# Performance work log

Measured on AMD Instinct MI355X. Metric: run time of the kernel, lower is better.

Reference implementation:

```python
import jax, jax.numpy as jnp
import numpy as np

N_NODES = 50000
N_EDGES = 800000


def setup_inputs() -> dict:
    key = jax.random.key(0)
    ks = jax.random.split(key, 9)
    d, h, hd = 128, 4, 32
    s = 1.0 / np.sqrt(d)
    return {
        "x": jax.random.normal(ks[0], (N_NODES, d), jnp.float32),
        "edge_index": jax.random.randint(ks[1], (2, N_EDGES), 0, N_NODES, jnp.int32),
        "W0": jax.random.normal(ks[2], (d, d), jnp.float32) * s,
        "att_l0": jax.random.normal(ks[3], (h, hd), jnp.float32) * s,
        "att_r0": jax.random.normal(ks[4], (h, hd), jnp.float32) * s,
        "b0": jnp.zeros((d,), jnp.float32),
        "W1": jax.random.normal(ks[5], (d, d), jnp.float32) * s,
        "att_l1": jax.random.normal(ks[6], (h, hd), jnp.float32) * s,
        "att_r1": jax.random.normal(ks[7], (h, hd), jnp.float32) * s,
        "b1": jnp.zeros((hd,), jnp.float32),
    }


def _gat_layer(x, src, dst, W, att_l, att_r, bias, concat):
    # x: [N, F_in]; W: [H*D, F_in] (torch Linear layout); att_*: [H, D]
    n = x.shape[0]
    h, d = att_l.shape
    hx = (x @ W.T).reshape(n, h, d)                     # [N,H,D]
    al = jnp.einsum('nhd,hd->nh', hx, att_l)            # [N,H]
    ar = jnp.einsum('nhd,hd->nh', hx, att_r)
    att = al[src] + ar[dst]                             # [E,H]
    att = jax.nn.leaky_relu(att, negative_slope=0.2)
    # segment softmax over destination nodes
    m = jax.ops.segment_max(att, dst, num_segments=n)   # [N,H]
    att = jnp.exp(att - m[dst])
    ssum = jax.ops.segment_sum(att, dst, num_segments=n)
    att = att / (ssum[dst] + 1e-9)                      # [E,H]
    msgs = att[:, :, None] * hx[src]                    # [E,H,D]
    out = jax.ops.segment_sum(msgs, dst, num_segments=n)  # [N,H,D]
    if concat:
        out = out.reshape(n, h * d)
    else:
        out = out.mean(axis=1)
    return out + bias


def reference(x, edge_index, W0, att_l0, att_r0, b0, W1, att_l1, att_r1, b1):
    src, dst = edge_index[0], edge_index[1]
    x = _gat_layer(x, src, dst, W0, att_l0, att_r0, b0, concat=True)
    x = jax.nn.relu(x)  # dropout is identity in eval mode
    x = _gat_layer(x, src, dst, W1, att_l1, att_r1, b1, concat=False)
    return x
```

## Files before the change

kernel.cpp:

```cpp
#include <hip/hip_runtime.h>
#include <hip/hip_bf16.h>

#define H 4
#define D 32
#define F 128
#define MAXDEG 64
#define PF 16

typedef __attribute__((ext_vector_type(8))) short bf16x8;
typedef __attribute__((ext_vector_type(4))) float f32x4;

__device__ __forceinline__ short f2bf(float v) {
    __hip_bfloat16 h = __float2bfloat16(v);
    return *reinterpret_cast<short*>(&h);
}
__device__ __forceinline__ float bf2f(short s) {
    __hip_bfloat16 h = *reinterpret_cast<__hip_bfloat16*>(&s);
    return __bfloat162float(h);
}

__device__ __forceinline__
void gemm_body(int bid, int nblocks, const float* __restrict__ X,
               const float* __restrict__ W, const float* __restrict__ attl,
               const float* __restrict__ attr, __hip_bfloat16* __restrict__ HXB,
               float* __restrict__ AL, float* __restrict__ AR, int ntiles) {
    const int wave = threadIdx.x >> 6;
    const int lane = threadIdx.x & 63;
    const int m    = lane & 15;
    const int q    = lane >> 4;
    const int q8   = q * 8;

    bf16x8 Bhi[2][4], Blo[2][4];
#pragma unroll
    for (int j = 0; j < 2; ++j) {
        const int fout = wave * 32 + j * 16 + m;
#pragma unroll
        for (int kc = 0; kc < 4; ++kc) {
            const float* wp = W + (size_t)fout * F + kc * 32 + q8;
            float4 w0 = *reinterpret_cast<const float4*>(wp);
            float4 w1 = *reinterpret_cast<const float4*>(wp + 4);
            float wv[8] = {w0.x, w0.y, w0.z, w0.w, w1.x, w1.y, w1.z, w1.w};
#pragma unroll
            for (int t = 0; t < 8; ++t) {
                short h = f2bf(wv[t]);
                Bhi[j][kc][t] = h;
                Blo[j][kc][t] = f2bf(wv[t] - bf2f(h));
            }
        }
    }
    const float alw0  = attl[wave * 32 + m];
    const float alw16 = attl[wave * 32 + 16 + m];
    const float arw0  = attr[wave * 32 + m];
    const float arw16 = attr[wave * 32 + 16 + m];

    for (int tile = bid; tile < ntiles; tile += nblocks) {
        const int node0 = tile * 16;
        bf16x8 Ahi[4], Alo[4];
        const float* xp = X + (size_t)(node0 + m) * F + q8;
#pragma unroll
        for (int kc = 0; kc < 4; ++kc) {
            float4 x0 = *reinterpret_cast<const float4*>(xp + kc * 32);
            float4 x1 = *reinterpret_cast<const float4*>(xp + kc * 32 + 4);
            float xv[8] = {x0.x, x0.y, x0.z, x0.w, x1.x, x1.y, x1.z, x1.w};
#pragma unroll
            for (int t = 0; t < 8; ++t) {
                short h = f2bf(xv[t]);
                Ahi[kc][t] = h;
                Alo[kc][t] = f2bf(xv[t] - bf2f(h));
            }
        }
        f32x4 acc0 = {0.f, 0.f, 0.f, 0.f};
        f32x4 acc1 = {0.f, 0.f, 0.f, 0.f};
#pragma unroll
        for (int kc = 0; kc < 4; ++kc) {
            acc0 = __builtin_amdgcn_mfma_f32_16x16x32_bf16(Ahi[kc], Bhi[0][kc], acc0, 0, 0, 0);
            acc1 = __builtin_amdgcn_mfma_f32_16x16x32_bf16(Ahi[kc], Bhi[1][kc], acc1, 0, 0, 0);
            acc0 = __builtin_amdgcn_mfma_f32_16x16x32_bf16(Ahi[kc], Blo[0][kc], acc0, 0, 0, 0);
            acc1 = __builtin_amdgcn_mfma_f32_16x16x32_bf16(Ahi[kc], Blo[1][kc], acc1, 0, 0, 0);
            acc0 = __builtin_amdgcn_mfma_f32_16x16x32_bf16(Alo[kc], Bhi[0][kc], acc0, 0, 0, 0);
            acc1 = __builtin_amdgcn_mfma_f32_16x16x32_bf16(Alo[kc], Bhi[1][kc], acc1, 0, 0, 0);
        }
        const int row0 = node0 + q * 4;
        const int col0 = wave * 32 + m;
#pragma unroll
        for (int r = 0; r < 4; ++r) {
            HXB[(size_t)(row0 + r) * F + col0]      = __float2bfloat16(acc0[r]);
            HXB[(size_t)(row0 + r) * F + col0 + 16] = __float2bfloat16(acc1[r]);
            float pal = acc0[r] * alw0 + acc1[r] * alw16;
            float par = acc0[r] * arw0 + acc1[r] * arw16;
#pragma unroll
            for (int o = 1; o < 16; o <<= 1) {
                pal += __shfl_xor(pal, o);
                par += __shfl_xor(par, o);
            }
            if (m == 0) {
                AL[(size_t)(row0 + r) * H + wave] = pal;
                AR[(size_t)(row0 + r) * H + wave] = par;
            }
        }
    }
}

__device__ __forceinline__
void wconv_body(const float* __restrict__ W1, __hip_bfloat16* __restrict__ W1hi,
                __hip_bfloat16* __restrict__ W1lo) {
    for (int i = threadIdx.x; i < F * F; i += 256) {
        float v = W1[i];
        short hi = f2bf(v);
        *reinterpret_cast<short*>(&W1hi[i]) = hi;
        *reinterpret_cast<short*>(&W1lo[i]) = f2bf(v - bf2f(hi));
    }
}

__device__ __forceinline__
void scatter_body(int sbid, const int* __restrict__ ei, int E,
                  int* __restrict__ deg, unsigned short* __restrict__ ssrc2u) {
    int base = (sbid * 256 + (int)threadIdx.x) * 4;
    if (base + 3 < E) {
        int4 s4 = *reinterpret_cast<const int4*>(ei + base);
        int4 d4 = *reinterpret_cast<const int4*>(ei + E + base);
        int s0 = atomicAdd(&deg[d4.x], 1);
        int s1 = atomicAdd(&deg[d4.y], 1);
        int s2 = atomicAdd(&deg[d4.z], 1);
        int s3 = atomicAdd(&deg[d4.w], 1);
        if (s0 < MAXDEG) ssrc2u[d4.x * MAXDEG + s0] = (unsigned short)s4.x;
        if (s1 < MAXDEG) ssrc2u[d4.y * MAXDEG + s1] = (unsigned short)s4.y;
        if (s2 < MAXDEG) ssrc2u[d4.z * MAXDEG + s2] = (unsigned short)s4.z;
        if (s3 < MAXDEG) ssrc2u[d4.w * MAXDEG + s3] = (unsigned short)s4.w;
    } else {
        for (int e = base; e < E; ++e) {
            int src = ei[e], dst = ei[E + e];
            int s = atomicAdd(&deg[dst], 1);
            if (s < MAXDEG) ssrc2u[dst * MAXDEG + s] = (unsigned short)src;
        }
    }
}

__global__ __launch_bounds__(256)
void k_pre(const float* __restrict__ X, const float* __restrict__ W0,
           const float* __restrict__ attl0, const float* __restrict__ attr0,
           __hip_bfloat16* __restrict__ HXB, float* __restrict__ AL,
           float* __restrict__ AR, int ntiles, int gemm_blocks,
           const float* __restrict__ W1, __hip_bfloat16* __restrict__ W1hi,
           __hip_bfloat16* __restrict__ W1lo,
           const int* __restrict__ ei, int E, int scatter_blocks,
           int* __restrict__ deg, unsigned short* __restrict__ ssrc2u) {
    const int bid = blockIdx.x;
    if (bid & 1) {
        const int s = bid >> 1;
        if (s < scatter_blocks) scatter_body(s, ei, E, deg, ssrc2u);
    } else {
        const int g = bid >> 1;
        if (g < gemm_blocks)
            gemm_body(g, gemm_blocks, X, W0, attl0, attr0, HXB, AL, AR, ntiles);
        else if (g == gemm_blocks)
            wconv_body(W1, W1hi, W1lo);
    }
}

__device__ __forceinline__
int stage_node(int g, int t, int n, const unsigned short* __restrict__ ssrc2u,
               const int* __restrict__ deg, const float* __restrict__ AL,
               const float4 ar4, int (*sidx)[MAXDEG], float (*sw)[MAXDEG][H]) {
    const int cnt  = min(deg[n], MAXDEG);
    const int rcnt = (cnt + PF - 1) & ~(PF - 1);
    if (t < rcnt) {
        if (t < cnt) {
            int s = ssrc2u[n * MAXDEG + t];
            sidx[g][t] = s;
            float4 al4 = *reinterpret_cast<const float4*>(AL + (size_t)s * H);
            float a0 = al4.x + ar4.x; a0 = a0 > 0.f ? a0 : 0.2f * a0;
            float a1 = al4.y + ar4.y; a1 = a1 > 0.f ? a1 : 0.2f * a1;
            float a2 = al4.z + ar4.z; a2 = a2 > 0.f ? a2 : 0.2f * a2;
            float a3 = al4.w + ar4.w; a3 = a3 > 0.f ? a3 : 0.2f * a3;
            sw[g][t][0] = __expf(a0);
            sw[g][t][1] = __expf(a1);
            sw[g][t][2] = __expf(a2);
            sw[g][t][3] = __expf(a3);
        } else {
            sidx[g][t] = 0;
            sw[g][t][0] = 0.f; sw[g][t][1] = 0.f; sw[g][t][2] = 0.f; sw[g][t][3] = 0.f;
        }
    }
    __builtin_amdgcn_wave_barrier();
    return rcnt;
}

__device__ __forceinline__
void gather_node(int g, int t, int h, int rcnt, const __hip_bfloat16* __restrict__ HXB,
                 const int (*sidx)[MAXDEG], const float (*sw)[MAXDEG][H],
                 float& accx, float& accy, float& wsum) {
    for (int base = 0; base < rcnt; base += PF) {
        __hip_bfloat162 v[PF];
#pragma unroll
        for (int j = 0; j < PF; ++j) {
            int s = sidx[g][base + j];
            v[j] = *reinterpret_cast<const __hip_bfloat162*>(HXB + (size_t)s * F + 2 * t);
        }
#pragma unroll
        for (int j = 0; j < PF; ++j) {
            float w = sw[g][base + j][h];
            float2 f = __bfloat1622float2(v[j]);
            accx += w * f.x;
            accy += w * f.y;
            wsum += w;
        }
    }
}

__global__ __launch_bounds__(256)
void k_aggr0(const unsigned short* __restrict__ ssrc2u, const int* __restrict__ deg,
             const float* __restrict__ AL, const float* __restrict__ AR,
             const __hip_bfloat16* __restrict__ HXB, const float* __restrict__ bias,
             float* __restrict__ out, int N) {
    __shared__ int   sidx[4][MAXDEG];
    __shared__ float sw[4][MAXDEG][H];
    const int g = threadIdx.x >> 6;
    const int t = threadIdx.x & 63;
    const int n = blockIdx.x * 4 + g;
    if (n >= N) return;
    const int h = t >> 4;
    const float4 ar4 = *reinterpret_cast<const float4*>(AR + (size_t)n * H);
    int rcnt = stage_node(g, t, n, ssrc2u, deg, AL, ar4, sidx, sw);
    float accx = 0.f, accy = 0.f, wsum = 0.f;
    gather_node(g, t, h, rcnt, HXB, sidx, sw, accx, accy, wsum);
    float inv = 1.f / (wsum + 1e-9f);
    float2 o;
    o.x = fmaxf(accx * inv + bias[2 * t], 0.f);
    o.y = fmaxf(accy * inv + bias[2 * t + 1], 0.f);
    *reinterpret_cast<float2*>(out + (size_t)n * F + 2 * t) = o;
}

__global__ __launch_bounds__(256)
void k_gemm1(const float* __restrict__ X, const __hip_bfloat16* __restrict__ W1hi,
             const __hip_bfloat16* __restrict__ W1lo,
             const float* __restrict__ attl, const float* __restrict__ attr,
             __hip_bfloat16* __restrict__ HXB, float* __restrict__ AL,
             float* __restrict__ AR, int ntiles) {
    const int wave = threadIdx.x >> 6;
    const int lane = threadIdx.x & 63;
    const int m    = lane & 15;
    const int q    = lane >> 4;
    const int q8   = q * 8;

    bf16x8 Bhi[2][4], Blo[2][4];
#pragma unroll
    for (int j = 0; j < 2; ++j) {
        const int fout = wave * 32 + j * 16 + m;
#pragma unroll
        for (int kc = 0; kc < 4; ++kc) {
            Bhi[j][kc] = *reinterpret_cast<const bf16x8*>(W1hi + (size_t)fout * F + kc * 32 + q8);
            Blo[j][kc] = *reinterpret_cast<const bf16x8*>(W1lo + (size_t)fout * F + kc * 32 + q8);
        }
    }
    const float alw0  = attl[wave * 32 + m];
    const float alw16 = attl[wave * 32 + 16 + m];
    const float arw0  = attr[wave * 32 + m];
    const float arw16 = attr[wave * 32 + 16 + m];

    for (int tile = blockIdx.x; tile < ntiles; tile += gridDim.x) {
        const int node0 = tile * 16;
        bf16x8 Ahi[4], Alo[4];
        const float* xp = X + (size_t)(node0 + m) * F + q8;
#pragma unroll
        for (int kc = 0; kc < 4; ++kc) {
            float4 x0 = *reinterpret_cast<const float4*>(xp + kc * 32);
            float4 x1 = *reinterpret_cast<const float4*>(xp + kc * 32 + 4);
            float xv[8] = {x0.x, x0.y, x0.z, x0.w, x1.x, x1.y, x1.z, x1.w};
#pragma unroll
            for (int t = 0; t < 8; ++t) {
                short h = f2bf(xv[t]);
                Ahi[kc][t] = h;
                Alo[kc][t] = f2bf(xv[t] - bf2f(h));
            }
        }
        f32x4 acc0 = {0.f, 0.f, 0.f, 0.f};
        f32x4 acc1 = {0.f, 0.f, 0.f, 0.f};
#pragma unroll
        for (int kc = 0; kc < 4; ++kc) {
            acc0 = __builtin_amdgcn_mfma_f32_16x16x32_bf16(Ahi[kc], Bhi[0][kc], acc0, 0, 0, 0);
            acc1 = __builtin_amdgcn_mfma_f32_16x16x32_bf16(Ahi[kc], Bhi[1][kc], acc1, 0, 0, 0);
            acc0 = __builtin_amdgcn_mfma_f32_16x16x32_bf16(Ahi[kc], Blo[0][kc], acc0, 0, 0, 0);
            acc1 = __builtin_amdgcn_mfma_f32_16x16x32_bf16(Ahi[kc], Blo[1][kc], acc1, 0, 0, 0);
            acc0 = __builtin_amdgcn_mfma_f32_16x16x32_bf16(Alo[kc], Bhi[0][kc], acc0, 0, 0, 0);
            acc1 = __builtin_amdgcn_mfma_f32_16x16x32_bf16(Alo[kc], Bhi[1][kc], acc1, 0, 0, 0);
        }
        const int row0 = node0 + q * 4;
        const int col0 = wave * 32 + m;
#pragma unroll
        for (int r = 0; r < 4; ++r) {
            HXB[(size_t)(row0 + r) * F + col0]      = __float2bfloat16(acc0[r]);
            HXB[(size_t)(row0 + r) * F + col0 + 16] = __float2bfloat16(acc1[r]);
            float pal = acc0[r] * alw0 + acc1[r] * alw16;
            float par = acc0[r] * arw0 + acc1[r] * arw16;
#pragma unroll
            for (int o = 1; o < 16; o <<= 1) {
                pal += __shfl_xor(pal, o);
                par += __shfl_xor(par, o);
            }
            if (m == 0) {
                AL[(size_t)(row0 + r) * H + wave] = pal;
                AR[(size_t)(row0 + r) * H + wave] = par;
            }
        }
    }
}

__global__ __launch_bounds__(256)
void k_aggr1(const unsigned short* __restrict__ ssrc2u, const int* __restrict__ deg,
             const float* __restrict__ AL, const float* __restrict__ AR,
             const __hip_bfloat16* __restrict__ HXB, const float* __restrict__ bias,
             float* __restrict__ out, int N) {
    __shared__ int   sidx[4][MAXDEG];
    __shared__ float sw[4][MAXDEG][H];
    const int g = threadIdx.x >> 6;
    const int t = threadIdx.x & 63;
    const int n = blockIdx.x * 4 + g;
    if (n >= N) return;
    const int h = t >> 4;
    const float4 ar4 = *reinterpret_cast<const float4*>(AR + (size_t)n * H);
    int rcnt = stage_node(g, t, n, ssrc2u, deg, AL, ar4, sidx, sw);
    float accx = 0.f, accy = 0.f, wsum = 0.f;
    gather_node(g, t, h, rcnt, HXB, sidx, sw, accx, accy, wsum);
    float inv = 1.f / (wsum + 1e-9f);
    float vx = accx * inv, vy = accy * inv;
    vx += __shfl_xor(vx, 16); vx += __shfl_xor(vx, 32);
    vy += __shfl_xor(vy, 16); vy += __shfl_xor(vy, 32);
    if (t < 16) {
        float2 o;
        o.x = 0.25f * vx + bias[2 * t];
        o.y = 0.25f * vy + bias[2 * t + 1];
        *reinterpret_cast<float2*>(out + (size_t)n * D + 2 * t) = o;
    }
}

extern "C" void kernel_launch(void* const* d_in, const int* in_sizes, int n_in,
                              void* d_out, int out_size, void* d_ws, size_t ws_size,
                              hipStream_t stream) {
    const float* x     = (const float*)d_in[0];
    const int*   ei    = (const int*)d_in[1];
    const float* W0    = (const float*)d_in[2];
    const float* attl0 = (const float*)d_in[3];
    const float* attr0 = (const float*)d_in[4];
    const float* b0    = (const float*)d_in[5];
    const float* W1    = (const float*)d_in[6];
    const float* attl1 = (const float*)d_in[7];
    const float* attr1 = (const float*)d_in[8];
    const float* b1    = (const float*)d_in[9];

    const int N = in_sizes[0] / F;
    const int E = in_sizes[1] / 2;
    const int ntiles = N / 16;

    char* p = (char*)d_ws;
    __hip_bfloat16* HXB  = (__hip_bfloat16*)p;  p += (size_t)N * F * 2;
    float* X1  = (float*)p;                     p += (size_t)N * F * 4;
    __hip_bfloat16* W1hi = (__hip_bfloat16*)p;  p += (size_t)F * F * 2;
    __hip_bfloat16* W1lo = (__hip_bfloat16*)p;  p += (size_t)F * F * 2;
    float* AL  = (float*)p;                     p += (size_t)N * H * 4;
    float* AR  = (float*)p;                     p += (size_t)N * H * 4;
    unsigned short* ssrc2u = (unsigned short*)p; p += (size_t)N * MAXDEG * 2;
    int* deg = (int*)p;

    hipMemsetAsync(deg, 0, (size_t)N * sizeof(int), stream);

    const int gemm_blocks    = 625;
    const int scatter_blocks = (E / 4 + 255) / 256;
    const int grid_pre = 2 * (scatter_blocks > gemm_blocks + 1 ? scatter_blocks
                                                               : gemm_blocks + 1);

    k_pre<<<grid_pre, 256, 0, stream>>>(x, W0, attl0, attr0, HXB, AL, AR,
                                        ntiles, gemm_blocks, W1, W1hi, W1lo,
                                        ei, E, scatter_blocks, deg, ssrc2u);

    k_aggr0<<<(N + 3) / 4, 256, 0, stream>>>(ssrc2u, deg, AL, AR, HXB, b0, X1, N);

    k_gemm1<<<gemm_blocks, 256, 0, stream>>>(X1, W1hi, W1lo, attl1, attr1,
                                             HXB, AL, AR, ntiles);

    k_aggr1<<<(N + 3) / 4, 256, 0, stream>>>(ssrc2u, deg, AL, AR, HXB, b1,
                                             (float*)d_out, N);
}
```

Baseline: 226.2 us.

## Gather two edges per wave with 8-byte loads and compact pre-kernel grid

The aggregation gather now splits each 64-lane wave into two halves that process alternate edges. Each lane loads 4 bf16 features (8 bytes) instead of 2, and the two halves are combined with a cross-half shuffle. This cuts the number of load instructions and doubles in-flight edges per wave, at the cost of an extra reduction and half the lanes sitting idle at the store. Separately, the fused pre-kernel replaces its interleaved block mapping, which launched idle blocks, with contiguous ranges: scatter blocks first, then GEMM blocks, then the weight-conversion block.

```diff
diff --git a/kernel.cpp b/kernel.cpp
--- a/kernel.cpp
+++ b/kernel.cpp
@@ -146,16 +146,13 @@
            const int* __restrict__ ei, int E, int scatter_blocks,
            int* __restrict__ deg, unsigned short* __restrict__ ssrc2u) {
     const int bid = blockIdx.x;
-    if (bid & 1) {
-        const int s = bid >> 1;
-        if (s < scatter_blocks) scatter_body(s, ei, E, deg, ssrc2u);
-    } else {
-        const int g = bid >> 1;
-        if (g < gemm_blocks)
-            gemm_body(g, gemm_blocks, X, W0, attl0, attr0, HXB, AL, AR, ntiles);
-        else if (g == gemm_blocks)
-            wconv_body(W1, W1hi, W1lo);
-    }
+    if (bid < scatter_blocks)
+        scatter_body(bid, ei, E, deg, ssrc2u);
+    else if (bid < scatter_blocks + gemm_blocks)
+        gemm_body(bid - scatter_blocks, gemm_blocks, X, W0, attl0, attr0,
+                  HXB, AL, AR, ntiles);
+    else
+        wconv_body(W1, W1hi, W1lo);
 }
 
 __device__ __forceinline__
@@ -187,25 +184,40 @@
 }
 
 __device__ __forceinline__
-void gather_node(int g, int t, int h, int rcnt, const __hip_bfloat16* __restrict__ HXB,
-                 const int (*sidx)[MAXDEG], const float (*sw)[MAXDEG][H],
-                 float& accx, float& accy, float& wsum) {
+void gather_node_pair(int g, int t, int rcnt, const __hip_bfloat16* __restrict__ HXB,
+                      const int (*sidx)[MAXDEG], const float (*sw)[MAXDEG][H],
+                      float4& acc, float& wsum) {
+    const int half = t >> 5;
+    const int fl   = t & 31;
+    const int h2   = fl >> 3;
     for (int base = 0; base < rcnt; base += PF) {
-        __hip_bfloat162 v[PF];
-#pragma unroll
-        for (int j = 0; j < PF; ++j) {
-            int s = sidx[g][base + j];
-            v[j] = *reinterpret_cast<const __hip_bfloat162*>(HXB + (size_t)s * F + 2 * t);
-        }
-#pragma unroll
-        for (int j = 0; j < PF; ++j) {
-            float w = sw[g][base + j][h];
-            float2 f = __bfloat1622float2(v[j]);
-            accx += w * f.x;
-            accy += w * f.y;
-            wsum += w;
-        }
-    }
+        float2 v[PF / 2];
+        float  w[PF / 2];
+#pragma unroll
+        for (int j = 0; j < PF / 2; ++j) {
+            int e = base + 2 * j + half;
+            int s = sidx[g][e];
+            v[j] = *reinterpret_cast<const float2*>(HXB + (size_t)s * F + 4 * fl);
+            w[j] = sw[g][e][h2];
+        }
+#pragma unroll
+        for (int j = 0; j < PF / 2; ++j) {
+            __hip_bfloat162 p0 = *reinterpret_cast<__hip_bfloat162*>(&v[j].x);
+            __hip_bfloat162 p1 = *reinterpret_cast<__hip_bfloat162*>(&v[j].y);
+            float2 f0 = __bfloat1622float2(p0);
+            float2 f1 = __bfloat1622float2(p1);
+            acc.x += w[j] * f0.x;
+            acc.y += w[j] * f0.y;
+            acc.z += w[j] * f1.x;
+            acc.w += w[j] * f1.y;
+            wsum  += w[j];
+        }
+    }
+    acc.x += __shfl_xor(acc.x, 32);
+    acc.y += __shfl_xor(acc.y, 32);
+    acc.z += __shfl_xor(acc.z, 32);
+    acc.w += __shfl_xor(acc.w, 32);
+    wsum  += __shfl_xor(wsum, 32);
 }
 
 __global__ __launch_bounds__(256)
@@ -219,16 +231,22 @@
     const int t = threadIdx.x & 63;
     const int n = blockIdx.x * 4 + g;
     if (n >= N) return;
-    const int h = t >> 4;
     const float4 ar4 = *reinterpret_cast<const float4*>(AR + (size_t)n * H);
     int rcnt = stage_node(g, t, n, ssrc2u, deg, AL, ar4, sidx, sw);
-    float accx = 0.f, accy = 0.f, wsum = 0.f;
-    gather_node(g, t, h, rcnt, HXB, sidx, sw, accx, accy, wsum);
-    float inv = 1.f / (wsum + 1e-9f);
-    float2 o;
-    o.x = fmaxf(accx * inv + bias[2 * t], 0.f);
-    o.y = fmaxf(accy * inv + bias[2 * t + 1], 0.f);
-    *reinterpret_cast<float2*>(out + (size_t)n * F + 2 * t) = o;
+    float4 acc = {0.f, 0.f, 0.f, 0.f};
+    float wsum = 0.f;
+    gather_node_pair(g, t, rcnt, HXB, sidx, sw, acc, wsum);
+    if (t < 32) {
+        const int fl = t;
+        float inv = 1.f / (wsum + 1e-9f);
+        float4 b = *reinterpret_cast<const float4*>(bias + 4 * fl);
+        float4 o;
+        o.x = fmaxf(acc.x * inv + b.x, 0.f);
+        o.y = fmaxf(acc.y * inv + b.y, 0.f);
+        o.z = fmaxf(acc.z * inv + b.z, 0.f);
+        o.w = fmaxf(acc.w * inv + b.w, 0.f);
+        *reinterpret_cast<float4*>(out + (size_t)n * F + 4 * fl) = o;
+    }
 }
 
 __global__ __launch_bounds__(256)
@@ -317,20 +335,26 @@
     const int t = threadIdx.x & 63;
     const int n = blockIdx.x * 4 + g;
     if (n >= N) return;
-    const int h = t >> 4;
     const float4 ar4 = *reinterpret_cast<const float4*>(AR + (size_t)n * H);
     int rcnt = stage_node(g, t, n, ssrc2u, deg, AL, ar4, sidx, sw);
-    float accx = 0.f, accy = 0.f, wsum = 0.f;
-    gather_node(g, t, h, rcnt, HXB, sidx, sw, accx, accy, wsum);
+    float4 acc = {0.f, 0.f, 0.f, 0.f};
+    float wsum = 0.f;
+    gather_node_pair(g, t, rcnt, HXB, sidx, sw, acc, wsum);
     float inv = 1.f / (wsum + 1e-9f);
-    float vx = accx * inv, vy = accy * inv;
-    vx += __shfl_xor(vx, 16); vx += __shfl_xor(vx, 32);
-    vy += __shfl_xor(vy, 16); vy += __shfl_xor(vy, 32);
-    if (t < 16) {
-        float2 o;
-        o.x = 0.25f * vx + bias[2 * t];
-        o.y = 0.25f * vy + bias[2 * t + 1];
-        *reinterpret_cast<float2*>(out + (size_t)n * D + 2 * t) = o;
+    float4 v;
+    v.x = acc.x * inv; v.y = acc.y * inv; v.z = acc.z * inv; v.w = acc.w * inv;
+    v.x += __shfl_xor(v.x, 8);  v.y += __shfl_xor(v.y, 8);
+    v.z += __shfl_xor(v.z, 8);  v.w += __shfl_xor(v.w, 8);
+    v.x += __shfl_xor(v.x, 16); v.y += __shfl_xor(v.y, 16);
+    v.z += __shfl_xor(v.z, 16); v.w += __shfl_xor(v.w, 16);
+    if (t < 8) {
+        float4 b = *reinterpret_cast<const float4*>(bias + 4 * t);
+        float4 o;
+        o.x = 0.25f * v.x + b.x;
+        o.y = 0.25f * v.y + b.y;
+        o.z = 0.25f * v.z + b.z;
+        o.w = 0.25f * v.w + b.w;
+        *reinterpret_cast<float4*>(out + (size_t)n * D + 4 * t) = o;
     }
 }
 
@@ -366,12 +390,10 @@
 
     const int gemm_blocks    = 625;
     const int scatter_blocks = (E / 4 + 255) / 256;
-    const int grid_pre = 2 * (scatter_blocks > gemm_blocks + 1 ? scatter_blocks
-                                                               : gemm_blocks + 1);
-
-    k_pre<<<grid_pre, 256, 0, stream>>>(x, W0, attl0, attr0, HXB, AL, AR,
-                                        ntiles, gemm_blocks, W1, W1hi, W1lo,
-                                        ei, E, scatter_blocks, deg, ssrc2u);
+
+    k_pre<<<scatter_blocks + gemm_blocks + 1, 256, 0, stream>>>(
+        x, W0, attl0, attr0, HXB, AL, AR, ntiles, gemm_blocks,
+        W1, W1hi, W1lo, ei, E, scatter_blocks, deg, ssrc2u);
 
     k_aggr0<<<(N + 3) / 4, 256, 0, stream>>>(ssrc2u, deg, AL, AR, HXB, b0, X1, N);
 
```

After: 234.8 us. 1.04x slower.

## Compute source attention logits on the fly from gathered features in aggregation

Applied to the files above, without the earlier changes.

Drops the precomputed AL array. The aggregation kernels now rebuild each edge's source logit by dotting the gathered bf16 feature row with att_l through a 16-lane shuffle reduction, instead of staging AL loads and exp weights in shared memory. This removes the AL writes in both GEMMs and the per-edge AL gather, at the cost of extra shuffles and redundant exp per lane. It also changes the k_pre block assignment from interleaved to contiguous GEMM/wconv/scatter ranges. Source logits now come from bf16-rounded features, which slightly changes numerics.

```diff
diff --git a/kernel.cpp b/kernel.cpp
--- a/kernel.cpp
+++ b/kernel.cpp
@@ -21,9 +21,9 @@
 
 __device__ __forceinline__
 void gemm_body(int bid, int nblocks, const float* __restrict__ X,
-               const float* __restrict__ W, const float* __restrict__ attl,
-               const float* __restrict__ attr, __hip_bfloat16* __restrict__ HXB,
-               float* __restrict__ AL, float* __restrict__ AR, int ntiles) {
+               const float* __restrict__ W, const float* __restrict__ attr,
+               __hip_bfloat16* __restrict__ HXB, float* __restrict__ AR,
+               int ntiles) {
     const int wave = threadIdx.x >> 6;
     const int lane = threadIdx.x & 63;
     const int m    = lane & 15;
@@ -48,8 +48,6 @@
             }
         }
     }
-    const float alw0  = attl[wave * 32 + m];
-    const float alw16 = attl[wave * 32 + 16 + m];
     const float arw0  = attr[wave * 32 + m];
     const float arw16 = attr[wave * 32 + 16 + m];
 
@@ -86,17 +84,12 @@
         for (int r = 0; r < 4; ++r) {
             HXB[(size_t)(row0 + r) * F + col0]      = __float2bfloat16(acc0[r]);
             HXB[(size_t)(row0 + r) * F + col0 + 16] = __float2bfloat16(acc1[r]);
-            float pal = acc0[r] * alw0 + acc1[r] * alw16;
             float par = acc0[r] * arw0 + acc1[r] * arw16;
 #pragma unroll
-            for (int o = 1; o < 16; o <<= 1) {
-                pal += __shfl_xor(pal, o);
+            for (int o = 1; o < 16; o <<= 1)
                 par += __shfl_xor(par, o);
-            }
-            if (m == 0) {
-                AL[(size_t)(row0 + r) * H + wave] = pal;
+            if (m == 0)
                 AR[(size_t)(row0 + r) * H + wave] = par;
-            }
         }
     }
 }
@@ -138,104 +131,88 @@
 
 __global__ __launch_bounds__(256)
 void k_pre(const float* __restrict__ X, const float* __restrict__ W0,
-           const float* __restrict__ attl0, const float* __restrict__ attr0,
-           __hip_bfloat16* __restrict__ HXB, float* __restrict__ AL,
+           const float* __restrict__ attr0, __hip_bfloat16* __restrict__ HXB,
            float* __restrict__ AR, int ntiles, int gemm_blocks,
            const float* __restrict__ W1, __hip_bfloat16* __restrict__ W1hi,
            __hip_bfloat16* __restrict__ W1lo,
-           const int* __restrict__ ei, int E, int scatter_blocks,
+           const int* __restrict__ ei, int E,
            int* __restrict__ deg, unsigned short* __restrict__ ssrc2u) {
     const int bid = blockIdx.x;
-    if (bid & 1) {
-        const int s = bid >> 1;
-        if (s < scatter_blocks) scatter_body(s, ei, E, deg, ssrc2u);
-    } else {
-        const int g = bid >> 1;
-        if (g < gemm_blocks)
-            gemm_body(g, gemm_blocks, X, W0, attl0, attr0, HXB, AL, AR, ntiles);
-        else if (g == gemm_blocks)
-            wconv_body(W1, W1hi, W1lo);
-    }
-}
-
-__device__ __forceinline__
-int stage_node(int g, int t, int n, const unsigned short* __restrict__ ssrc2u,
-               const int* __restrict__ deg, const float* __restrict__ AL,
-               const float4 ar4, int (*sidx)[MAXDEG], float (*sw)[MAXDEG][H]) {
-    const int cnt  = min(deg[n], MAXDEG);
-    const int rcnt = (cnt + PF - 1) & ~(PF - 1);
-    if (t < rcnt) {
-        if (t < cnt) {
-            int s = ssrc2u[n * MAXDEG + t];
-            sidx[g][t] = s;
-            float4 al4 = *reinterpret_cast<const float4*>(AL + (size_t)s * H);
-            float a0 = al4.x + ar4.x; a0 = a0 > 0.f ? a0 : 0.2f * a0;
-            float a1 = al4.y + ar4.y; a1 = a1 > 0.f ? a1 : 0.2f * a1;
-            float a2 = al4.z + ar4.z; a2 = a2 > 0.f ? a2 : 0.2f * a2;
-            float a3 = al4.w + ar4.w; a3 = a3 > 0.f ? a3 : 0.2f * a3;
-            sw[g][t][0] = __expf(a0);
-            sw[g][t][1] = __expf(a1);
-            sw[g][t][2] = __expf(a2);
-            sw[g][t][3] = __expf(a3);
-        } else {
-            sidx[g][t] = 0;
-            sw[g][t][0] = 0.f; sw[g][t][1] = 0.f; sw[g][t][2] = 0.f; sw[g][t][3] = 0.f;
-        }
-    }
-    __builtin_amdgcn_wave_barrier();
-    return rcnt;
-}
-
-__device__ __forceinline__
-void gather_node(int g, int t, int h, int rcnt, const __hip_bfloat16* __restrict__ HXB,
-                 const int (*sidx)[MAXDEG], const float (*sw)[MAXDEG][H],
-                 float& accx, float& accy, float& wsum) {
-    for (int base = 0; base < rcnt; base += PF) {
-        __hip_bfloat162 v[PF];
-#pragma unroll
-        for (int j = 0; j < PF; ++j) {
-            int s = sidx[g][base + j];
-            v[j] = *reinterpret_cast<const __hip_bfloat162*>(HXB + (size_t)s * F + 2 * t);
-        }
-#pragma unroll
-        for (int j = 0; j < PF; ++j) {
-            float w = sw[g][base + j][h];
-            float2 f = __bfloat1622float2(v[j]);
-            accx += w * f.x;
-            accy += w * f.y;
-            wsum += w;
-        }
-    }
-}
-
+    if (bid < gemm_blocks)
+        gemm_body(bid, gemm_blocks, X, W0, attr0, HXB, AR, ntiles);
+    else if (bid == gemm_blocks)
+        wconv_body(W1, W1hi, W1lo);
+    else
+        scatter_body(bid - gemm_blocks - 1, ei, E, deg, ssrc2u);
+}
+
+template<int MODE>
 __global__ __launch_bounds__(256)
-void k_aggr0(const unsigned short* __restrict__ ssrc2u, const int* __restrict__ deg,
-             const float* __restrict__ AL, const float* __restrict__ AR,
-             const __hip_bfloat16* __restrict__ HXB, const float* __restrict__ bias,
-             float* __restrict__ out, int N) {
-    __shared__ int   sidx[4][MAXDEG];
-    __shared__ float sw[4][MAXDEG][H];
+void k_aggr(const unsigned short* __restrict__ ssrc2u, const int* __restrict__ deg,
+            const float* __restrict__ AR, const __hip_bfloat16* __restrict__ HXB,
+            const float* __restrict__ attl, const float* __restrict__ bias,
+            float* __restrict__ out, int N) {
+    __shared__ unsigned short sidx[4][MAXDEG];
     const int g = threadIdx.x >> 6;
     const int t = threadIdx.x & 63;
     const int n = blockIdx.x * 4 + g;
     if (n >= N) return;
     const int h = t >> 4;
+    const float alw0 = attl[2 * t];
+    const float alw1 = attl[2 * t + 1];
     const float4 ar4 = *reinterpret_cast<const float4*>(AR + (size_t)n * H);
-    int rcnt = stage_node(g, t, n, ssrc2u, deg, AL, ar4, sidx, sw);
+    const float arh = (h == 0) ? ar4.x : (h == 1) ? ar4.y : (h == 2) ? ar4.z : ar4.w;
+    const int cnt = min(deg[n], MAXDEG);
+    sidx[g][t] = (t < cnt) ? ssrc2u[n * MAXDEG + t] : (unsigned short)0;
+    __builtin_amdgcn_wave_barrier();
     float accx = 0.f, accy = 0.f, wsum = 0.f;
-    gather_node(g, t, h, rcnt, HXB, sidx, sw, accx, accy, wsum);
+    const int rcnt = (cnt + PF - 1) & ~(PF - 1);
+    for (int base = 0; base < rcnt; base += PF) {
+        float2 v[PF];
+#pragma unroll
+        for (int j = 0; j < PF; ++j) {
+            int s = sidx[g][base + j];
+            v[j] = __bfloat1622float2(
+                *reinterpret_cast<const __hip_bfloat162*>(HXB + (size_t)s * F + 2 * t));
+        }
+#pragma unroll
+        for (int j = 0; j < PF; ++j) {
+            float p = v[j].x * alw0 + v[j].y * alw1;
+            p += __shfl_xor(p, 1);
+            p += __shfl_xor(p, 2);
+            p += __shfl_xor(p, 4);
+            p += __shfl_xor(p, 8);
+            float a = p + arh;
+            a = a > 0.f ? a : 0.2f * a;
+            float w = (base + j < cnt) ? __expf(a) : 0.f;
+            accx += w * v[j].x;
+            accy += w * v[j].y;
+            wsum += w;
+        }
+    }
     float inv = 1.f / (wsum + 1e-9f);
-    float2 o;
-    o.x = fmaxf(accx * inv + bias[2 * t], 0.f);
-    o.y = fmaxf(accy * inv + bias[2 * t + 1], 0.f);
-    *reinterpret_cast<float2*>(out + (size_t)n * F + 2 * t) = o;
+    float vx = accx * inv, vy = accy * inv;
+    if (MODE == 0) {
+        float2 o;
+        o.x = fmaxf(vx + bias[2 * t], 0.f);
+        o.y = fmaxf(vy + bias[2 * t + 1], 0.f);
+        *reinterpret_cast<float2*>(out + (size_t)n * F + 2 * t) = o;
+    } else {
+        vx += __shfl_xor(vx, 16); vx += __shfl_xor(vx, 32);
+        vy += __shfl_xor(vy, 16); vy += __shfl_xor(vy, 32);
+        if (t < 16) {
+            float2 o;
+            o.x = 0.25f * vx + bias[2 * t];
+            o.y = 0.25f * vy + bias[2 * t + 1];
+            *reinterpret_cast<float2*>(out + (size_t)n * D + 2 * t) = o;
+        }
+    }
 }
 
 __global__ __launch_bounds__(256)
 void k_gemm1(const float* __restrict__ X, const __hip_bfloat16* __restrict__ W1hi,
              const __hip_bfloat16* __restrict__ W1lo,
-             const float* __restrict__ attl, const float* __restrict__ attr,
-             __hip_bfloat16* __restrict__ HXB, float* __restrict__ AL,
+             const float* __restrict__ attr, __hip_bfloat16* __restrict__ HXB,
              float* __restrict__ AR, int ntiles) {
     const int wave = threadIdx.x >> 6;
     const int lane = threadIdx.x & 63;
@@ -253,8 +230,6 @@
             Blo[j][kc] = *reinterpret_cast<const bf16x8*>(W1lo + (size_t)fout * F + kc * 32 + q8);
         }
     }
-    const float alw0  = attl[wave * 32 + m];
-    const float alw16 = attl[wave * 32 + 16 + m];
     const float arw0  = attr[wave * 32 + m];
     const float arw16 = attr[wave * 32 + 16 + m];
 
@@ -291,46 +266,13 @@
         for (int r = 0; r < 4; ++r) {
             HXB[(size_t)(row0 + r) * F + col0]      = __float2bfloat16(acc0[r]);
             HXB[(size_t)(row0 + r) * F + col0 + 16] = __float2bfloat16(acc1[r]);
-            float pal = acc0[r] * alw0 + acc1[r] * alw16;
             float par = acc0[r] * arw0 + acc1[r] * arw16;
 #pragma unroll
-            for (int o = 1; o < 16; o <<= 1) {
-                pal += __shfl_xor(pal, o);
+            for (int o = 1; o < 16; o <<= 1)
                 par += __shfl_xor(par, o);
-            }
-            if (m == 0) {
-                AL[(size_t)(row0 + r) * H + wave] = pal;
+            if (m == 0)
                 AR[(size_t)(row0 + r) * H + wave] = par;
-            }
-        }
-    }
-}
-
-__global__ __launch_bounds__(256)
-void k_aggr1(const unsigned short* __restrict__ ssrc2u, const int* __restrict__ deg,
-             const float* __restrict__ AL, const float* __restrict__ AR,
-             const __hip_bfloat16* __restrict__ HXB, const float* __restrict__ bias,
-             float* __restrict__ out, int N) {
-    __shared__ int   sidx[4][MAXDEG];
-    __shared__ float sw[4][MAXDEG][H];
-    const int g = threadIdx.x >> 6;
-    const int t = threadIdx.x & 63;
-    const int n = blockIdx.x * 4 + g;
-    if (n >= N) return;
-    const int h = t >> 4;
-    const float4 ar4 = *reinterpret_cast<const float4*>(AR + (size_t)n * H);
-    int rcnt = stage_node(g, t, n, ssrc2u, deg, AL, ar4, sidx, sw);
-    float accx = 0.f, accy = 0.f, wsum = 0.f;
-    gather_node(g, t, h, rcnt, HXB, sidx, sw, accx, accy, wsum);
-    float inv = 1.f / (wsum + 1e-9f);
-    float vx = accx * inv, vy = accy * inv;
-    vx += __shfl_xor(vx, 16); vx += __shfl_xor(vx, 32);
-    vy += __shfl_xor(vy, 16); vy += __shfl_xor(vy, 32);
-    if (t < 16) {
-        float2 o;
-        o.x = 0.25f * vx + bias[2 * t];
-        o.y = 0.25f * vy + bias[2 * t + 1];
-        *reinterpret_cast<float2*>(out + (size_t)n * D + 2 * t) = o;
+        }
     }
 }
 
@@ -357,7 +299,6 @@
     float* X1  = (float*)p;                     p += (size_t)N * F * 4;
     __hip_bfloat16* W1hi = (__hip_bfloat16*)p;  p += (size_t)F * F * 2;
     __hip_bfloat16* W1lo = (__hip_bfloat16*)p;  p += (size_t)F * F * 2;
-    float* AL  = (float*)p;                     p += (size_t)N * H * 4;
     float* AR  = (float*)p;                     p += (size_t)N * H * 4;
     unsigned short* ssrc2u = (unsigned short*)p; p += (size_t)N * MAXDEG * 2;
     int* deg = (int*)p;
@@ -366,18 +307,17 @@
 
     const int gemm_blocks    = 625;
     const int scatter_blocks = (E / 4 + 255) / 256;
-    const int grid_pre = 2 * (scatter_blocks > gemm_blocks + 1 ? scatter_blocks
-                                                               : gemm_blocks + 1);
-
-    k_pre<<<grid_pre, 256, 0, stream>>>(x, W0, attl0, attr0, HXB, AL, AR,
-                                        ntiles, gemm_blocks, W1, W1hi, W1lo,
-                                        ei, E, scatter_blocks, deg, ssrc2u);
-
-    k_aggr0<<<(N + 3) / 4, 256, 0, stream>>>(ssrc2u, deg, AL, AR, HXB, b0, X1, N);
-
-    k_gemm1<<<gemm_blocks, 256, 0, stream>>>(X1, W1hi, W1lo, attl1, attr1,
-                                             HXB, AL, AR, ntiles);
-
-    k_aggr1<<<(N + 3) / 4, 256, 0, stream>>>(ssrc2u, deg, AL, AR, HXB, b1,
-                                             (float*)d_out, N);
-}
+
+    k_pre<<<gemm_blocks + 1 + scatter_blocks, 256, 0, stream>>>(
+        x, W0, attr0, HXB, AR, ntiles, gemm_blocks,
+        W1, W1hi, W1lo, ei, E, deg, ssrc2u);
+
+    k_aggr<0><<<(N + 3) / 4, 256, 0, stream>>>(ssrc2u, deg, AR, HXB, attl0, b0,
+                                               X1, N);
+
+    k_gemm1<<<gemm_blocks, 256, 0, stream>>>(X1, W1hi, W1lo, attr1, HXB, AR,
+                                             ntiles);
+
+    k_aggr<1><<<(N + 3) / 4, 256, 0, stream>>>(ssrc2u, deg, AR, HXB, attl1, b1,
+                                               (float*)d_out, N);
+}
```

New measurement: 299.9 us. +32.6%, slower.

## Replace global-atomic CSR scatter with two-pass bucketed binning

Applied to the files above, without the earlier changes.

The edge scatter changes from one global atomic per edge on the degree array into a two-pass scheme. First, edges are binned into 256 destination buckets using shared-memory counters and packed src/local-dst records. Then a separate kernel builds the per-node source lists with shared atomics. This aims to cut global atomic contention and scattered writes, at the cost of an extra kernel launch and an intermediate buffer with a fixed per-bucket capacity (CAP=4096), which can overflow if a bucket receives more than its expected ~3136 edges. The per-node degree memset is dropped because the second kernel writes deg directly.

```diff
diff --git a/kernel.cpp b/kernel.cpp
--- a/kernel.cpp
+++ b/kernel.cpp
@@ -6,6 +6,9 @@
 #define F 128
 #define MAXDEG 64
 #define PF 16
+#define NBUCK 256
+#define BUCKW 196
+#define CAP   4096
 
 typedef __attribute__((ext_vector_type(8))) short bf16x8;
 typedef __attribute__((ext_vector_type(4))) float f32x4;
@@ -113,26 +116,30 @@
 }
 
 __device__ __forceinline__
-void scatter_body(int sbid, const int* __restrict__ ei, int E,
-                  int* __restrict__ deg, unsigned short* __restrict__ ssrc2u) {
-    int base = (sbid * 256 + (int)threadIdx.x) * 4;
-    if (base + 3 < E) {
-        int4 s4 = *reinterpret_cast<const int4*>(ei + base);
-        int4 d4 = *reinterpret_cast<const int4*>(ei + E + base);
-        int s0 = atomicAdd(&deg[d4.x], 1);
-        int s1 = atomicAdd(&deg[d4.y], 1);
-        int s2 = atomicAdd(&deg[d4.z], 1);
-        int s3 = atomicAdd(&deg[d4.w], 1);
-        if (s0 < MAXDEG) ssrc2u[d4.x * MAXDEG + s0] = (unsigned short)s4.x;
-        if (s1 < MAXDEG) ssrc2u[d4.y * MAXDEG + s1] = (unsigned short)s4.y;
-        if (s2 < MAXDEG) ssrc2u[d4.z * MAXDEG + s2] = (unsigned short)s4.z;
-        if (s3 < MAXDEG) ssrc2u[d4.w * MAXDEG + s3] = (unsigned short)s4.w;
-    } else {
-        for (int e = base; e < E; ++e) {
-            int src = ei[e], dst = ei[E + e];
-            int s = atomicAdd(&deg[dst], 1);
-            if (s < MAXDEG) ssrc2u[dst * MAXDEG + s] = (unsigned short)src;
-        }
+void bucketA_body(int abid, int nablk, const int* __restrict__ ei, int E,
+                  int* __restrict__ gcnt, unsigned int* __restrict__ buf) {
+    __shared__ int lcnt[NBUCK];
+    __shared__ int lpos[NBUCK];
+    const int tid = threadIdx.x;
+    lcnt[tid] = 0;
+    __syncthreads();
+    const int per = E / nablk;
+    const int e0 = abid * per;
+    const int e1 = (abid == nablk - 1) ? E : e0 + per;
+    for (int e = e0 + tid; e < e1; e += 256)
+        atomicAdd(&lcnt[ei[E + e] / BUCKW], 1);
+    __syncthreads();
+    if (lcnt[tid] > 0)
+        lpos[tid] = atomicAdd(&gcnt[tid], lcnt[tid]);
+    __syncthreads();
+    for (int e = e0 + tid; e < e1; e += 256) {
+        int src = ei[e];
+        int dst = ei[E + e];
+        int b = dst / BUCKW;
+        int pos = atomicAdd(&lpos[b], 1);
+        if (pos < CAP)
+            buf[(size_t)b * CAP + pos] =
+                (unsigned)src | ((unsigned)(dst - b * BUCKW) << 16);
     }
 }
 
@@ -143,18 +150,38 @@
            float* __restrict__ AR, int ntiles, int gemm_blocks,
            const float* __restrict__ W1, __hip_bfloat16* __restrict__ W1hi,
            __hip_bfloat16* __restrict__ W1lo,
-           const int* __restrict__ ei, int E, int scatter_blocks,
-           int* __restrict__ deg, unsigned short* __restrict__ ssrc2u) {
+           const int* __restrict__ ei, int E, int nablk,
+           int* __restrict__ gcnt, unsigned int* __restrict__ buf) {
     const int bid = blockIdx.x;
-    if (bid & 1) {
-        const int s = bid >> 1;
-        if (s < scatter_blocks) scatter_body(s, ei, E, deg, ssrc2u);
-    } else {
-        const int g = bid >> 1;
-        if (g < gemm_blocks)
-            gemm_body(g, gemm_blocks, X, W0, attl0, attr0, HXB, AL, AR, ntiles);
-        else if (g == gemm_blocks)
-            wconv_body(W1, W1hi, W1lo);
+    if (bid < gemm_blocks)
+        gemm_body(bid, gemm_blocks, X, W0, attl0, attr0, HXB, AL, AR, ntiles);
+    else if (bid == gemm_blocks)
+        wconv_body(W1, W1hi, W1lo);
+    else
+        bucketA_body(bid - gemm_blocks - 1, nablk, ei, E, gcnt, buf);
+}
+
+__global__ __launch_bounds__(256)
+void k_bucket(const unsigned int* __restrict__ buf, const int* __restrict__ gcnt,
+              int* __restrict__ deg, unsigned short* __restrict__ ssrc2u, int N) {
+    __shared__ int cnt[BUCKW];
+    const int b = blockIdx.x;
+    const int tid = threadIdx.x;
+    if (tid < BUCKW) cnt[tid] = 0;
+    __syncthreads();
+    const int m = min(gcnt[b], CAP);
+    for (int i = tid; i < m; i += 256) {
+        unsigned rec = buf[(size_t)b * CAP + i];
+        int src  = rec & 0xffff;
+        int ldst = rec >> 16;
+        int slot = atomicAdd(&cnt[ldst], 1);
+        if (slot < MAXDEG)
+            ssrc2u[(size_t)(b * BUCKW + ldst) * MAXDEG + slot] = (unsigned short)src;
+    }
+    __syncthreads();
+    if (tid < BUCKW) {
+        int node = b * BUCKW + tid;
+        if (node < N) deg[node] = cnt[tid];
     }
 }
 
@@ -351,6 +378,7 @@
     const int N = in_sizes[0] / F;
     const int E = in_sizes[1] / 2;
     const int ntiles = N / 16;
+    const int nablk  = 128;
 
     char* p = (char*)d_ws;
     __hip_bfloat16* HXB  = (__hip_bfloat16*)p;  p += (size_t)N * F * 2;
@@ -360,18 +388,19 @@
     float* AL  = (float*)p;                     p += (size_t)N * H * 4;
     float* AR  = (float*)p;                     p += (size_t)N * H * 4;
     unsigned short* ssrc2u = (unsigned short*)p; p += (size_t)N * MAXDEG * 2;
-    int* deg = (int*)p;
-
-    hipMemsetAsync(deg, 0, (size_t)N * sizeof(int), stream);
-
-    const int gemm_blocks    = 625;
-    const int scatter_blocks = (E / 4 + 255) / 256;
-    const int grid_pre = 2 * (scatter_blocks > gemm_blocks + 1 ? scatter_blocks
-                                                               : gemm_blocks + 1);
-
-    k_pre<<<grid_pre, 256, 0, stream>>>(x, W0, attl0, attr0, HXB, AL, AR,
-                                        ntiles, gemm_blocks, W1, W1hi, W1lo,
-                                        ei, E, scatter_blocks, deg, ssrc2u);
+    int* deg = (int*)p;                         p += (size_t)N * 4;
+    unsigned int* buf = (unsigned int*)p;       p += (size_t)NBUCK * CAP * 4;
+    int* gcnt = (int*)p;
+
+    hipMemsetAsync(gcnt, 0, NBUCK * sizeof(int), stream);
+
+    const int gemm_blocks = 625;
+
+    k_pre<<<gemm_blocks + 1 + nablk, 256, 0, stream>>>(
+        x, W0, attl0, attr0, HXB, AL, AR, ntiles, gemm_blocks,
+        W1, W1hi, W1lo, ei, E, nablk, gcnt, buf);
+
+    k_bucket<<<NBUCK, 256, 0, stream>>>(buf, gcnt, deg, ssrc2u, N);
 
     k_aggr0<<<(N + 3) / 4, 256, 0, stream>>>(ssrc2u, deg, AL, AR, HXB, b0, X1, N);
 
```

New measurement: 215.0 us. 4.9% less time.
